# Kernel tuning notes

Measured on AMD Instinct MI355X. Metric: run time of the kernel, lower is better.

## Reference

```python
import jax, jax.numpy as jnp
import numpy as np

C_CONST = 8.0   # RG-LRU decay constant (Griffin/Hawk)
EPS = 1e-6      # RMSNorm eps
K = 4           # causal depthwise conv kernel size


def rmsnorm(x, w):
    # x: [B,S,D]
    var = jnp.mean(x * x, axis=-1, keepdims=True)
    return x * jax.lax.rsqrt(var + EPS) * w


def causal_depthwise_conv(x, conv_w, conv_b):
    # x: [B,S,D], conv_w: [K,D], conv_b: [D]; causal (left-pad K-1)
    B, S, D = x.shape
    xp = jnp.pad(x, ((0, 0), (K - 1, 0), (0, 0)))
    out = conv_b
    for k in range(K):  # tiny fixed loop over kernel taps
        out = out + conv_w[k] * xp[:, k:k + S, :]
    return out


def rg_lru(x, Wi, Wa, lam):
    # x: [B,S,D]; diagonal linear recurrence h_t = a_t*h_{t-1} + sqrt(1-a_t^2)*(i_t*x_t)
    r = jax.nn.sigmoid(jnp.einsum('bsd,de->bse', x, Wa))   # recurrence gate
    i = jax.nn.sigmoid(jnp.einsum('bsd,de->bse', x, Wi))   # input gate
    log_a = -C_CONST * jax.nn.softplus(lam) * r            # [B,S,D]
    a = jnp.exp(log_a)
    b = jnp.sqrt(jnp.maximum(1.0 - a * a, 1e-12)) * (i * x)

    def comb(e1, e2):
        a1, b1 = e1
        a2, b2 = e2
        return (a1 * a2, a2 * b1 + b2)

    _, h = jax.lax.associative_scan(comb, (a, b), axis=1)
    return h


def setup_inputs() -> dict:
    key = jax.random.key(0)
    ks = jax.random.split(key, 16)
    B, S, D, H = 4, 2048, 1024, 4096
    s = 0.02
    return {
        'x': jax.random.normal(ks[0], (B, S, D), jnp.float32),
        'norm1_w': jnp.ones((D,), jnp.float32),
        'Wx': jax.random.normal(ks[1], (D, D), jnp.float32) * s,
        'Wy': jax.random.normal(ks[2], (D, D), jnp.float32) * s,
        'conv_w': jax.random.normal(ks[3], (K, D), jnp.float32) * s,
        'conv_b': jnp.zeros((D,), jnp.float32),
        'Wi': jax.random.normal(ks[4], (D, D), jnp.float32) * s,
        'Wa': jax.random.normal(ks[5], (D, D), jnp.float32) * s,
        'lam': jax.random.normal(ks[6], (D,), jnp.float32) * 0.5,
        'Wo': jax.random.normal(ks[7], (D, D), jnp.float32) * s,
        'norm2_w': jnp.ones((D,), jnp.float32),
        'Wg': jax.random.normal(ks[8], (D, H), jnp.float32) * s,
        'Wu': jax.random.normal(ks[9], (D, H), jnp.float32) * s,
        'Wd': jax.random.normal(ks[10], (H, D), jnp.float32) * s,
    }


def reference(x, norm1_w, Wx, Wy, conv_w, conv_b, Wi, Wa, lam, Wo,
              norm2_w, Wg, Wu, Wd):
    # --- mixing block (Hawk recurrent block) with pre-norm + residual ---
    t = rmsnorm(x, norm1_w)
    xb = jnp.einsum('bsd,de->bse', t, Wx)          # recurrence branch
    xb = causal_depthwise_conv(xb, conv_w, conv_b)
    h = rg_lru(xb, Wi, Wa, lam)
    yb = jax.nn.gelu(jnp.einsum('bsd,de->bse', t, Wy))  # gate branch
    mix = jnp.einsum('bsd,de->bse', h * yb, Wo)
    h1 = x + mix
    # --- gated MLP with pre-norm + residual ---
    u = rmsnorm(h1, norm2_w)
    ffn = jnp.einsum('bsh,hd->bsd', jax.nn.gelu(jnp.einsum('bsd,dh->bsh', u, Wg)) * jnp.einsum('bsd,dh->bsh', u, Wu), Wd)
    return h1 + ffn
```

## Files before the change

kernel.cpp:

```cpp
#include <hip/hip_runtime.h>
#include <hip/hip_bf16.h>
#include <stdint.h>

#define B_SZ   4
#define S_LEN  2048
#define D_DIM  1024
#define H_DIM  4096
#define T_TOK  (B_SZ * S_LEN)
#define NC     64
#define CL     32

typedef unsigned short u16;
typedef unsigned int   u32;
typedef __attribute__((ext_vector_type(8))) short short8;
typedef __attribute__((ext_vector_type(4))) float f32x4;

__device__ __forceinline__ float tof(u16 u) {
    union { u32 i; float f; } v; v.i = ((u32)u) << 16; return v.f;
}
__device__ __forceinline__ u16 tobf(float f) {
    union { float f; u32 i; } v; v.f = f;
    u32 x = v.i;
    return (u16)((x + 0x7FFFu + ((x >> 16) & 1u)) >> 16);
}
__device__ __forceinline__ void unp8(uint4 v, float* f) {
    f[0] = tof(v.x & 0xffff); f[1] = tof(v.x >> 16);
    f[2] = tof(v.y & 0xffff); f[3] = tof(v.y >> 16);
    f[4] = tof(v.z & 0xffff); f[5] = tof(v.z >> 16);
    f[6] = tof(v.w & 0xffff); f[7] = tof(v.w >> 16);
}

__device__ __forceinline__ float gelu_f(float x) {
    float x3 = x * x * x;
    float tin = 0.7978845608028654f * (x + 0.044715f * x3);
    float e = __expf(2.f * tin);
    float th = 1.f - 2.f / (e + 1.f);
    return 0.5f * x * (1.f + th);
}
__device__ __forceinline__ float sig_f(float x) {
    return 1.f / (1.f + __expf(-x));
}

__device__ __forceinline__ void gload16(const void* g, void* l) {
    __builtin_amdgcn_global_load_lds(
        (const __attribute__((address_space(1))) u32*)g,
        (__attribute__((address_space(3))) u32*)l,
        16, 0, 0);
}

__global__ void detect_k(const u32* __restrict__ w, int* __restrict__ flag) {
    if (blockIdx.x == 0 && threadIdx.x == 0)
        *flag = (w[0] == 0x3F800000u) ? 1 : 0;
}

__global__ __launch_bounds__(256) void prep_small(
    const void* n1w, const void* n2w, const void* cw, const void* cb,
    const void* lam, u16* n1wc, u16* n2wc, u16* cwc, u16* cbc,
    float* acoef, const int* __restrict__ flagp) {
    int i = blockIdx.x * 256 + threadIdx.x;
    bool f32 = (*flagp) != 0;
    auto rd = [&](const void* p, int j) {
        return f32 ? ((const float*)p)[j] : tof(((const u16*)p)[j]);
    };
    if (i < 1024) n1wc[i] = tobf(rd(n1w, i));
    else if (i < 2048) n2wc[i - 1024] = tobf(rd(n2w, i - 1024));
    else if (i < 6144) cwc[i - 2048] = tobf(rd(cw, i - 2048));
    else if (i < 7168) cbc[i - 6144] = tobf(rd(cb, i - 6144));
    else {
        int d = i - 7168;
        float l = rd(lam, d);
        float sp = fmaxf(l, 0.f) + log1pf(__expf(-fabsf(l)));
        acoef[d] = -8.f * sp;
    }
}

__global__ __launch_bounds__(256) void transpose_any(
    const void* __restrict__ W, u16* __restrict__ WT, int R, int C,
    const int* __restrict__ flag) {
    __shared__ u16 tile[32][33];
    bool f32 = (*flag) != 0;
    int tx = threadIdx.x & 31, ty = threadIdx.x >> 5;
    int c0 = blockIdx.x * 32, r0 = blockIdx.y * 32;
#pragma unroll
    for (int k = 0; k < 4; k++) {
        size_t idx = (size_t)(r0 + ty + k * 8) * C + c0 + tx;
        tile[ty + k * 8][tx] = f32 ? tobf(((const float*)W)[idx])
                                   : ((const u16*)W)[idx];
    }
    __syncthreads();
#pragma unroll
    for (int k = 0; k < 4; k++)
        WT[(size_t)(c0 + ty + k * 8) * R + r0 + tx] = tile[tx][ty + k * 8];
}

__global__ __launch_bounds__(256) void transpose_ilv(
    const void* __restrict__ W, u16* __restrict__ WT, int R, int C, int par,
    const int* __restrict__ flag) {
    __shared__ u16 tile[32][33];
    bool f32 = (*flag) != 0;
    int tx = threadIdx.x & 31, ty = threadIdx.x >> 5;
    int c0 = blockIdx.x * 32, r0 = blockIdx.y * 32;
#pragma unroll
    for (int k = 0; k < 4; k++) {
        size_t idx = (size_t)(r0 + ty + k * 8) * C + c0 + tx;
        tile[ty + k * 8][tx] = f32 ? tobf(((const float*)W)[idx])
                                   : ((const u16*)W)[idx];
    }
    __syncthreads();
#pragma unroll
    for (int k = 0; k < 4; k++)
        WT[(size_t)(2 * (c0 + ty + k * 8) + par) * R + r0 + tx] =
            tile[tx][ty + k * 8];
}

__global__ __launch_bounds__(256) void rmsnorm_any(
    const void* __restrict__ X, const u16* __restrict__ Wt, u16* __restrict__ O,
    const int* __restrict__ flagp, int in_mode) {
    bool f32 = in_mode == 1 || (*flagp != 0);
    int row = blockIdx.x;
    int t = threadIdx.x;
    float x0, x1, x2, x3;
    if (f32) {
        float4 v = ((const float4*)((const float*)X + (size_t)row * D_DIM))[t];
        x0 = v.x; x1 = v.y; x2 = v.z; x3 = v.w;
    } else {
        uint2 pv = ((const uint2*)((const u16*)X + (size_t)row * D_DIM))[t];
        x0 = tof(pv.x & 0xffff); x1 = tof(pv.x >> 16);
        x2 = tof(pv.y & 0xffff); x3 = tof(pv.y >> 16);
    }
    float ss = x0 * x0 + x1 * x1 + x2 * x2 + x3 * x3;
#pragma unroll
    for (int off = 32; off; off >>= 1) ss += __shfl_down(ss, off, 64);
    __shared__ float red[4];
    if ((t & 63) == 0) red[t >> 6] = ss;
    __syncthreads();
    float tot = red[0] + red[1] + red[2] + red[3];
    float rs = rsqrtf(tot * (1.f / D_DIM) + 1e-6f);
    uint2 wv = ((const uint2*)Wt)[t];
    float w0 = tof(wv.x & 0xffff), w1 = tof(wv.x >> 16);
    float w2 = tof(wv.y & 0xffff), w3 = tof(wv.y >> 16);
    uint2 ov;
    ov.x = (u32)tobf(x0 * rs * w0) | ((u32)tobf(x1 * rs * w1) << 16);
    ov.y = (u32)tobf(x2 * rs * w2) | ((u32)tobf(x3 * rs * w3) << 16);
    ((uint2*)(O + (size_t)row * D_DIM))[t] = ov;
}

__global__ __launch_bounds__(256) void conv_k(
    const u16* __restrict__ xb, const u16* __restrict__ cw,
    const u16* __restrict__ cb, u16* __restrict__ xc) {
    size_t idx = (size_t)blockIdx.x * 256 + threadIdx.x;
    int dp = (int)(idx & 127);
    size_t ts = idx >> 7;
    int s = (int)(ts & (S_LEN - 1));
    int d0 = dp * 8;
    float acc[8];
    unp8(*(const uint4*)(cb + d0), acc);
    size_t base = ts * D_DIM + d0;
#pragma unroll
    for (int k = 0; k < 4; k++) {
        int sp = s + k - 3;
        if (sp >= 0) {
            float xf[8], wf[8];
            unp8(*(const uint4*)(xb + base + (ptrdiff_t)(k - 3) * D_DIM), xf);
            unp8(*(const uint4*)(cw + k * D_DIM + d0), wf);
#pragma unroll
            for (int e = 0; e < 8; e++) acc[e] += wf[e] * xf[e];
        }
    }
    uint4 ov;
    ov.x = (u32)tobf(acc[0]) | ((u32)tobf(acc[1]) << 16);
    ov.y = (u32)tobf(acc[2]) | ((u32)tobf(acc[3]) << 16);
    ov.z = (u32)tobf(acc[4]) | ((u32)tobf(acc[5]) << 16);
    ov.w = (u32)tobf(acc[6]) | ((u32)tobf(acc[7]) << 16);
    *(uint4*)(xc + base) = ov;
}

__global__ __launch_bounds__(256) void gates_chunk_k(
    const u16* __restrict__ r, const u16* __restrict__ ii, const u16* __restrict__ xc,
    const float* __restrict__ acoef, float2* __restrict__ Ap2, float2* __restrict__ Bs2) {
    int d2 = blockIdx.x * 256 + threadIdx.x;
    int c = blockIdx.y, b = blockIdx.z;
    float ac0 = acoef[d2 * 2], ac1 = acoef[d2 * 2 + 1];
    const u32* r2 = (const u32*)r;
    const u32* i2 = (const u32*)ii;
    const u32* x2 = (const u32*)xc;
    size_t base = ((size_t)b * S_LEN + c * CL) * (D_DIM / 2) + d2;
    float ap0 = 1.f, bs0 = 0.f, ap1 = 1.f, bs1 = 0.f;
    for (int tt = 0; tt < CL; tt++) {
        u32 rv = r2[base], iv = i2[base], xv = x2[base];
        float a0 = __expf(ac0 * tof(rv & 0xffff));
        float a1 = __expf(ac1 * tof(rv >> 16));
        float b0 = sqrtf(fmaxf(1.f - a0 * a0, 1e-12f)) * (tof(iv & 0xffff) * tof(xv & 0xffff));
        float b1 = sqrtf(fmaxf(1.f - a1 * a1, 1e-12f)) * (tof(iv >> 16) * tof(xv >> 16));
        ap0 *= a0; bs0 = fmaf(a0, bs0, b0);
        ap1 *= a1; bs1 = fmaf(a1, bs1, b1);
        base += D_DIM / 2;
    }
    size_t o = ((size_t)b * NC + c) * (D_DIM / 2) + d2;
    Ap2[o] = make_float2(ap0, ap1);
    Bs2[o] = make_float2(bs0, bs1);
}

__global__ __launch_bounds__(256) void carry_k(
    const float2* __restrict__ Ap2, const float2* __restrict__ Bs2,
    float2* __restrict__ carry2) {
    int d2 = blockIdx.x * 256 + threadIdx.x;
    int b = blockIdx.y;
    float2 h = make_float2(0.f, 0.f);
    for (int c = 0; c < NC; c++) {
        size_t o = ((size_t)b * NC + c) * (D_DIM / 2) + d2;
        float2 ap = Ap2[o], bs = Bs2[o];
        carry2[o] = h;
        h.x = fmaf(ap.x, h.x, bs.x);
        h.y = fmaf(ap.y, h.y, bs.y);
    }
}

__global__ __launch_bounds__(256) void apply_k(
    const u16* __restrict__ r, const u16* __restrict__ ii, const u16* __restrict__ xc,
    const float* __restrict__ acoef, const float2* __restrict__ carry2,
    const u16* __restrict__ yb, u16* __restrict__ g) {
    int d2 = blockIdx.x * 256 + threadIdx.x;
    int c = blockIdx.y, b = blockIdx.z;
    float ac0 = acoef[d2 * 2], ac1 = acoef[d2 * 2 + 1];
    float2 h = carry2[((size_t)b * NC + c) * (D_DIM / 2) + d2];
    const u32* r2 = (const u32*)r;
    const u32* i2 = (const u32*)ii;
    const u32* x2 = (const u32*)xc;
    const u32* y2 = (const u32*)yb;
    u32* g2 = (u32*)g;
    size_t base = ((size_t)b * S_LEN + c * CL) * (D_DIM / 2) + d2;
    for (int tt = 0; tt < CL; tt++) {
        u32 rv = r2[base], iv = i2[base], xv = x2[base], yv = y2[base];
        float a0 = __expf(ac0 * tof(rv & 0xffff));
        float a1 = __expf(ac1 * tof(rv >> 16));
        float b0 = sqrtf(fmaxf(1.f - a0 * a0, 1e-12f)) * (tof(iv & 0xffff) * tof(xv & 0xffff));
        float b1 = sqrtf(fmaxf(1.f - a1 * a1, 1e-12f)) * (tof(iv >> 16) * tof(xv >> 16));
        h.x = fmaf(a0, h.x, b0);
        h.y = fmaf(a1, h.y, b1);
        g2[base] = (u32)tobf(h.x * tof(yv & 0xffff)) |
                   ((u32)tobf(h.y * tof(yv >> 16)) << 16);
        base += D_DIM / 2;
    }
}

enum { EPI_NONE = 0, EPI_GELU = 1, EPI_SIG = 2, EPI_RESID = 3, EPI_MUL = 4 };

template <int E>
__device__ __forceinline__ float epi_apply(float v, const void* aux, size_t idx,
                                           bool auxF32) {
    if (E == EPI_GELU) return gelu_f(v);
    if (E == EPI_SIG) return sig_f(v);
    if (E == EPI_RESID) {
        float a = auxF32 ? ((const float*)aux)[idx] : tof(((const u16*)aux)[idx]);
        return v + a;
    }
    if (E == EPI_MUL) {
        float a = auxF32 ? ((const float*)aux)[idx] : tof(((const u16*)aux)[idx]);
        return v * a;
    }
    return v;
}

#define BK 64

template <int BM, int BN, int WMD, int WND, int EPI0, int EPI1, bool OUTF32,
          bool SWZ, bool GLU>
__global__ __launch_bounds__(WMD * WND * 64, 2) void gemm_db(
    const u16* __restrict__ A, const u16* __restrict__ BT,
    void* __restrict__ C0v, void* __restrict__ C1v, const void* __restrict__ aux,
    const int* __restrict__ flagp, int aux_mode,
    int M, int N, int K, int halfN) {
    constexpr int T  = WMD * WND * 64;
    constexpr int MR = BM / WMD;
    constexpr int NR = BN / WND;
    constexpr int MI = MR / 16;
    constexpr int NJ = NR / 16;
    constexpr int RPR = T / 8;

    __shared__ __align__(16) u16 As[2][BM * BK];
    __shared__ __align__(16) u16 Bs[2][BN * BK];

    const int t = threadIdx.x;
    const int lane = t & 63;
    const int w = t >> 6;
    const int wm = w / WND, wn = w % WND;
    const int quad = lane >> 4, l16 = lane & 15;

    int mt, nt;
    if (SWZ) {
        int GN = gridDim.x;
        int L = blockIdx.y * GN + blockIdx.x;
        int per = (GN * gridDim.y) >> 3;
        int id = (L & 7) * per + (L >> 3);
        mt = id / GN; nt = id - mt * GN;
    } else {
        mt = blockIdx.y; nt = blockIdx.x;
    }
    const int m0 = mt * BM;
    const int n0 = nt * BN;

    const int srow = t >> 3;
    const int cbg  = (t & 7) ^ (srow & 7);
    const u16* ag = A + (size_t)(m0 + srow) * K + cbg * 8;
    const u16* bg = BT + (size_t)(n0 + srow) * K + cbg * 8;
    const size_t rstep = (size_t)RPR * K;

    f32x4 acc[MI][NJ];
#pragma unroll
    for (int i = 0; i < MI; i++)
#pragma unroll
        for (int j = 0; j < NJ; j++) acc[i][j] = (f32x4){0.f, 0.f, 0.f, 0.f};

    const int r7 = l16 & 7;

    auto STAGE = [&](int s, int kt) {
        const u16* a = ag + (size_t)kt * BK;
        const u16* b = bg + (size_t)kt * BK;
        char* lA = (char*)&As[s][0] + t * 16;
        char* lB = (char*)&Bs[s][0] + t * 16;
#pragma unroll
        for (int rr = 0; rr < BM / RPR; rr++)
            gload16(a + rr * rstep, lA + rr * (RPR * 128));
#pragma unroll
        for (int rr = 0; rr < BN / RPR; rr++)
            gload16(b + rr * rstep, lB + rr * (RPR * 128));
    };
    auto COMPUTE = [&](int s) {
#pragma unroll
        for (int kk = 0; kk < 2; kk++) {
            const int cb = ((kk * 4 + quad) ^ r7) * 8;
            short8 af[MI], bf[NJ];
#pragma unroll
            for (int i = 0; i < MI; i++)
                af[i] = *(const short8*)&As[s][(wm * MR + i * 16 + l16) * BK + cb];
#pragma unroll
            for (int j = 0; j < NJ; j++)
                bf[j] = *(const short8*)&Bs[s][(wn * NR + j * 16 + l16) * BK + cb];
#pragma unroll
            for (int i = 0; i < MI; i++)
#pragma unroll
                for (int j = 0; j < NJ; j++)
                    acc[i][j] = __builtin_amdgcn_mfma_f32_16x16x32_bf16(
                        af[i], bf[j], acc[i][j], 0, 0, 0);
        }
    };

    const int NT = K >> 6;
    STAGE(0, 0);
    __syncthreads();
    for (int kt = 0; kt < NT; kt += 2) {
        STAGE(1, kt + 1);
        COMPUTE(0);
        __syncthreads();
        if (kt + 2 < NT) STAGE(0, kt + 2);
        COMPUTE(1);
        __syncthreads();
    }

    const bool auxF32 = (aux_mode == 2) || (aux_mode == 1 && *flagp != 0);
    const int side = (!GLU && n0 >= halfN) ? 1 : 0;
    void* Cv = side ? C1v : C0v;

#pragma unroll
    for (int i = 0; i < MI; i++) {
        int mbase = m0 + wm * MR + i * 16 + quad * 4;
#pragma unroll
        for (int j = 0; j < NJ; j++) {
            int ncol = n0 - side * halfN + wn * NR + j * 16 + l16;
#pragma unroll
            for (int rr = 0; rr < 4; rr++) {
                float v = acc[i][j][rr];
                if (GLU) {
                    float o = __shfl_xor(v, 1);
                    bool odd = (l16 & 1) != 0;
                    float gg = odd ? o : v;
                    float uu = odd ? v : o;
                    float res = gelu_f(gg) * uu;
                    if (!odd)
                        ((u16*)C0v)[(size_t)(mbase + rr) * halfN + (ncol >> 1)]
                            = tobf(res);
                } else {
                    size_t idx = (size_t)(mbase + rr) * halfN + ncol;
                    v = side ? epi_apply<EPI1>(v, aux, idx, auxF32)
                             : epi_apply<EPI0>(v, aux, idx, auxF32);
                    if (OUTF32) ((float*)Cv)[idx] = v;
                    else        ((u16*)Cv)[idx] = tobf(v);
                }
            }
        }
    }
}

extern "C" void kernel_launch(void* const* d_in, const int* in_sizes, int n_in,
                              void* d_out, int out_size, void* d_ws, size_t ws_size,
                              hipStream_t stream) {
    const void* x      = d_in[0];
    const void* n1w    = d_in[1];
    const void* Wx     = d_in[2];
    const void* Wy     = d_in[3];
    const void* conv_w = d_in[4];
    const void* conv_b = d_in[5];
    const void* Wi     = d_in[6];
    const void* Wa     = d_in[7];
    const void* lam    = d_in[8];
    const void* Wo     = d_in[9];
    const void* n2w    = d_in[10];
    const void* Wg     = d_in[11];
    const void* Wu     = d_in[12];
    const void* Wd     = d_in[13];
    float* out = (float*)d_out;

    char* ws = (char*)d_ws;
    auto alloc = [&](size_t bytes) {
        char* p = ws;
        ws += (bytes + 255) & ~(size_t)255;
        return p;
    };
    const size_t DD = (size_t)D_DIM * D_DIM;
    const size_t DH = (size_t)D_DIM * H_DIM * 2;
    const size_t TD = (size_t)T_TOK * D_DIM * 2;
    const size_t TH = (size_t)T_TOK * H_DIM * 2;

    int*  dflag  = (int*)alloc(256);
    u16*  n1wc   = (u16*)alloc(D_DIM * 2);
    u16*  n2wc   = (u16*)alloc(D_DIM * 2);
    u16*  cwc    = (u16*)alloc(4 * D_DIM * 2);
    u16*  cbc    = (u16*)alloc(D_DIM * 2);
    float* acoef = (float*)alloc(D_DIM * 4);
    float2* Ap2    = (float2*)alloc((size_t)B_SZ * NC * D_DIM * 4);
    float2* Bs2    = (float2*)alloc((size_t)B_SZ * NC * D_DIM * 4);
    float2* carry2 = (float2*)alloc((size_t)B_SZ * NC * D_DIM * 4);
    u16* WT  = (u16*)alloc(2 * DH);
    u16* T0  = (u16*)alloc(TD);
    u16* T1  = (u16*)alloc(TD);
    u16* T2  = (u16*)alloc(TD);
    u16* T3  = (u16*)alloc(TD);
    u16* T4  = (u16*)alloc(TD);
    u16* ggb = (u16*)alloc(TH);
    float* h1f = (float*)alloc((size_t)T_TOK * D_DIM * 4);

    dim3 b256(256);

    detect_k<<<dim3(1), dim3(64), 0, stream>>>((const u32*)n1w, dflag);
    prep_small<<<dim3(32), b256, 0, stream>>>(n1w, n2w, conv_w, conv_b, lam,
                                              n1wc, n2wc, cwc, cbc, acoef, dflag);

    rmsnorm_any<<<dim3(T_TOK), b256, 0, stream>>>(x, n1wc, T2, dflag, 0);

    transpose_any<<<dim3(32, 32), b256, 0, stream>>>(Wx, WT, D_DIM, D_DIM, dflag);
    transpose_any<<<dim3(32, 32), b256, 0, stream>>>(Wy, WT + DD, D_DIM, D_DIM, dflag);
    gemm_db<128, 128, 2, 2, EPI_NONE, EPI_GELU, false, false, false>
        <<<dim3(2 * D_DIM / 128, T_TOK / 128), b256, 0, stream>>>(
        T2, WT, T1, T3, nullptr, dflag, 0, T_TOK, 2 * D_DIM, D_DIM, D_DIM);

    conv_k<<<dim3(T_TOK * D_DIM / 8 / 256), b256, 0, stream>>>(T1, cwc, cbc, T0);

    transpose_any<<<dim3(32, 32), b256, 0, stream>>>(Wa, WT, D_DIM, D_DIM, dflag);
    transpose_any<<<dim3(32, 32), b256, 0, stream>>>(Wi, WT + DD, D_DIM, D_DIM, dflag);
    gemm_db<128, 128, 2, 2, EPI_SIG, EPI_SIG, false, false, false>
        <<<dim3(2 * D_DIM / 128, T_TOK / 128), b256, 0, stream>>>(
        T0, WT, T4, T2, nullptr, dflag, 0, T_TOK, 2 * D_DIM, D_DIM, D_DIM);

    gates_chunk_k<<<dim3(2, NC, B_SZ), b256, 0, stream>>>(T4, T2, T0, acoef, Ap2, Bs2);
    carry_k<<<dim3(2, B_SZ), b256, 0, stream>>>(Ap2, Bs2, carry2);
    apply_k<<<dim3(2, NC, B_SZ), b256, 0, stream>>>(T4, T2, T0, acoef, carry2, T3, T4);

    transpose_any<<<dim3(32, 32), b256, 0, stream>>>(Wo, WT, D_DIM, D_DIM, dflag);
    gemm_db<128, 128, 2, 2, EPI_RESID, EPI_RESID, true, false, false>
        <<<dim3(D_DIM / 128, T_TOK / 128), b256, 0, stream>>>(
        T4, WT, h1f, h1f, x, dflag, 1, T_TOK, D_DIM, D_DIM, D_DIM);

    rmsnorm_any<<<dim3(T_TOK), b256, 0, stream>>>(h1f, n2wc, T1, dflag, 1);

    transpose_ilv<<<dim3(H_DIM / 32, D_DIM / 32), b256, 0, stream>>>(
        Wg, WT, D_DIM, H_DIM, 0, dflag);
    transpose_ilv<<<dim3(H_DIM / 32, D_DIM / 32), b256, 0, stream>>>(
        Wu, WT, D_DIM, H_DIM, 1, dflag);
    gemm_db<128, 128, 2, 2, EPI_NONE, EPI_NONE, false, false, true>
        <<<dim3(2 * H_DIM / 128, T_TOK / 128), b256, 0, stream>>>(
        T1, WT, ggb, ggb, nullptr, dflag, 0, T_TOK, 2 * H_DIM, D_DIM, H_DIM);

    transpose_any<<<dim3(32, 128), b256, 0, stream>>>(Wd, WT, H_DIM, D_DIM, dflag);
    gemm_db<128, 128, 2, 2, EPI_RESID, EPI_RESID, true, true, false>
        <<<dim3(D_DIM / 128, T_TOK / 128), b256, 0, stream>>>(
        ggb, WT, out, out, h1f, dflag, 2, T_TOK, D_DIM, H_DIM, D_DIM);
}
```

Before: 685.9 us.

## Merge weight transposes into one launch and halve GEMM K-tile for higher occupancy

All eight weight transposes now run in a single launch that writes to separate workspace buffers, replacing eight small launches interleaved with the GEMMs. The GEMM K-tile drops from 64 to 32, with a new LDS swizzle and a single MFMA k-step per stage, which halves shared memory per block. Launch bounds are raised to 4 blocks per CU to use that. The cost is twice as many barriers and loop iterations per GEMM, less work per synchronisation, and possible register spills under the tighter bound.

```diff
diff --git a/kernel.cpp b/kernel.cpp
--- a/kernel.cpp
+++ b/kernel.cpp
@@ -74,13 +74,27 @@
     }
 }
 
-__global__ __launch_bounds__(256) void transpose_any(
-    const void* __restrict__ W, u16* __restrict__ WT, int R, int C,
-    const int* __restrict__ flag) {
+__global__ __launch_bounds__(256) void transpose_all(
+    const void* Wx_, const void* Wy_, const void* Wa_, const void* Wi_,
+    const void* Wo_, const void* Wd_, const void* Wg_, const void* Wu_,
+    u16* WTxy, u16* WTai, u16* WTo, u16* WTd, u16* WTgu,
+    const int* __restrict__ flagp) {
+    const size_t DD = (size_t)D_DIM * D_DIM;
+    bool f32 = (*flagp) != 0;
+    int b = blockIdx.x;
+    const void* W; u16* WT; int R, C, gx, ilv = 0, par = 0;
+    if (b < 1024)       { W = Wx_; WT = WTxy;      R = 1024; C = 1024; gx = 32;  b -= 0; }
+    else if (b < 2048)  { W = Wy_; WT = WTxy + DD; R = 1024; C = 1024; gx = 32;  b -= 1024; }
+    else if (b < 3072)  { W = Wa_; WT = WTai;      R = 1024; C = 1024; gx = 32;  b -= 2048; }
+    else if (b < 4096)  { W = Wi_; WT = WTai + DD; R = 1024; C = 1024; gx = 32;  b -= 3072; }
+    else if (b < 5120)  { W = Wo_; WT = WTo;       R = 1024; C = 1024; gx = 32;  b -= 4096; }
+    else if (b < 9216)  { W = Wd_; WT = WTd;       R = 4096; C = 1024; gx = 32;  b -= 5120; }
+    else if (b < 13312) { W = Wg_; WT = WTgu;      R = 1024; C = 4096; gx = 128; b -= 9216;  ilv = 1; par = 0; }
+    else                { W = Wu_; WT = WTgu;      R = 1024; C = 4096; gx = 128; b -= 13312; ilv = 1; par = 1; }
+    int bx = b % gx, by = b / gx;
     __shared__ u16 tile[32][33];
-    bool f32 = (*flag) != 0;
     int tx = threadIdx.x & 31, ty = threadIdx.x >> 5;
-    int c0 = blockIdx.x * 32, r0 = blockIdx.y * 32;
+    int c0 = bx * 32, r0 = by * 32;
 #pragma unroll
     for (int k = 0; k < 4; k++) {
         size_t idx = (size_t)(r0 + ty + k * 8) * C + c0 + tx;
@@ -89,28 +103,11 @@
     }
     __syncthreads();
 #pragma unroll
-    for (int k = 0; k < 4; k++)
-        WT[(size_t)(c0 + ty + k * 8) * R + r0 + tx] = tile[tx][ty + k * 8];
-}
-
-__global__ __launch_bounds__(256) void transpose_ilv(
-    const void* __restrict__ W, u16* __restrict__ WT, int R, int C, int par,
-    const int* __restrict__ flag) {
-    __shared__ u16 tile[32][33];
-    bool f32 = (*flag) != 0;
-    int tx = threadIdx.x & 31, ty = threadIdx.x >> 5;
-    int c0 = blockIdx.x * 32, r0 = blockIdx.y * 32;
-#pragma unroll
     for (int k = 0; k < 4; k++) {
-        size_t idx = (size_t)(r0 + ty + k * 8) * C + c0 + tx;
-        tile[ty + k * 8][tx] = f32 ? tobf(((const float*)W)[idx])
-                                   : ((const u16*)W)[idx];
-    }
-    __syncthreads();
-#pragma unroll
-    for (int k = 0; k < 4; k++)
-        WT[(size_t)(2 * (c0 + ty + k * 8) + par) * R + r0 + tx] =
-            tile[tx][ty + k * 8];
+        int cc = c0 + ty + k * 8;
+        size_t orow = ilv ? (size_t)(2 * cc + par) : (size_t)cc;
+        WT[orow * R + r0 + tx] = tile[tx][ty + k * 8];
+    }
 }
 
 __global__ __launch_bounds__(256) void rmsnorm_any(
@@ -262,11 +259,11 @@
     return v;
 }
 
-#define BK 64
+#define BK 32
 
 template <int BM, int BN, int WMD, int WND, int EPI0, int EPI1, bool OUTF32,
           bool SWZ, bool GLU>
-__global__ __launch_bounds__(WMD * WND * 64, 2) void gemm_db(
+__global__ __launch_bounds__(WMD * WND * 64, 4) void gemm_db(
     const u16* __restrict__ A, const u16* __restrict__ BT,
     void* __restrict__ C0v, void* __restrict__ C1v, const void* __restrict__ aux,
     const int* __restrict__ flagp, int aux_mode,
@@ -276,7 +273,7 @@
     constexpr int NR = BN / WND;
     constexpr int MI = MR / 16;
     constexpr int NJ = NR / 16;
-    constexpr int RPR = T / 8;
+    constexpr int RPR = T / 4;
 
     __shared__ __align__(16) u16 As[2][BM * BK];
     __shared__ __align__(16) u16 Bs[2][BN * BK];
@@ -300,8 +297,8 @@
     const int m0 = mt * BM;
     const int n0 = nt * BN;
 
-    const int srow = t >> 3;
-    const int cbg  = (t & 7) ^ (srow & 7);
+    const int srow = t >> 2;
+    const int cbg  = (t & 3) ^ ((srow >> 1) & 3);
     const u16* ag = A + (size_t)(m0 + srow) * K + cbg * 8;
     const u16* bg = BT + (size_t)(n0 + srow) * K + cbg * 8;
     const size_t rstep = (size_t)RPR * K;
@@ -312,7 +309,7 @@
 #pragma unroll
         for (int j = 0; j < NJ; j++) acc[i][j] = (f32x4){0.f, 0.f, 0.f, 0.f};
 
-    const int r7 = l16 & 7;
+    const int pcb = (quad ^ ((l16 >> 1) & 3)) * 8;
 
     auto STAGE = [&](int s, int kt) {
         const u16* a = ag + (size_t)kt * BK;
@@ -321,32 +318,28 @@
         char* lB = (char*)&Bs[s][0] + t * 16;
 #pragma unroll
         for (int rr = 0; rr < BM / RPR; rr++)
-            gload16(a + rr * rstep, lA + rr * (RPR * 128));
+            gload16(a + rr * rstep, lA + rr * (RPR * 64));
 #pragma unroll
         for (int rr = 0; rr < BN / RPR; rr++)
-            gload16(b + rr * rstep, lB + rr * (RPR * 128));
+            gload16(b + rr * rstep, lB + rr * (RPR * 64));
     };
     auto COMPUTE = [&](int s) {
-#pragma unroll
-        for (int kk = 0; kk < 2; kk++) {
-            const int cb = ((kk * 4 + quad) ^ r7) * 8;
-            short8 af[MI], bf[NJ];
-#pragma unroll
-            for (int i = 0; i < MI; i++)
-                af[i] = *(const short8*)&As[s][(wm * MR + i * 16 + l16) * BK + cb];
+        short8 af[MI], bf[NJ];
+#pragma unroll
+        for (int i = 0; i < MI; i++)
+            af[i] = *(const short8*)&As[s][(wm * MR + i * 16 + l16) * BK + pcb];
+#pragma unroll
+        for (int j = 0; j < NJ; j++)
+            bf[j] = *(const short8*)&Bs[s][(wn * NR + j * 16 + l16) * BK + pcb];
+#pragma unroll
+        for (int i = 0; i < MI; i++)
 #pragma unroll
             for (int j = 0; j < NJ; j++)
-                bf[j] = *(const short8*)&Bs[s][(wn * NR + j * 16 + l16) * BK + cb];
-#pragma unroll
-            for (int i = 0; i < MI; i++)
-#pragma unroll
-                for (int j = 0; j < NJ; j++)
-                    acc[i][j] = __builtin_amdgcn_mfma_f32_16x16x32_bf16(
-                        af[i], bf[j], acc[i][j], 0, 0, 0);
-        }
+                acc[i][j] = __builtin_amdgcn_mfma_f32_16x16x32_bf16(
+                    af[i], bf[j], acc[i][j], 0, 0, 0);
     };
 
-    const int NT = K >> 6;
+    const int NT = K >> 5;
     STAGE(0, 0);
     __syncthreads();
     for (int kt = 0; kt < NT; kt += 2) {
@@ -418,7 +411,6 @@
         return p;
     };
     const size_t DD = (size_t)D_DIM * D_DIM;
-    const size_t DH = (size_t)D_DIM * H_DIM * 2;
     const size_t TD = (size_t)T_TOK * D_DIM * 2;
     const size_t TH = (size_t)T_TOK * H_DIM * 2;
 
@@ -431,7 +423,11 @@
     float2* Ap2    = (float2*)alloc((size_t)B_SZ * NC * D_DIM * 4);
     float2* Bs2    = (float2*)alloc((size_t)B_SZ * NC * D_DIM * 4);
     float2* carry2 = (float2*)alloc((size_t)B_SZ * NC * D_DIM * 4);
-    u16* WT  = (u16*)alloc(2 * DH);
+    u16* WTxy = (u16*)alloc(2 * DD * 2);
+    u16* WTai = (u16*)alloc(2 * DD * 2);
+    u16* WTo  = (u16*)alloc(DD * 2);
+    u16* WTd  = (u16*)alloc((size_t)D_DIM * H_DIM * 2);
+    u16* WTgu = (u16*)alloc((size_t)D_DIM * H_DIM * 2 * 2);
     u16* T0  = (u16*)alloc(TD);
     u16* T1  = (u16*)alloc(TD);
     u16* T2  = (u16*)alloc(TD);
@@ -445,44 +441,36 @@
     detect_k<<<dim3(1), dim3(64), 0, stream>>>((const u32*)n1w, dflag);
     prep_small<<<dim3(32), b256, 0, stream>>>(n1w, n2w, conv_w, conv_b, lam,
                                               n1wc, n2wc, cwc, cbc, acoef, dflag);
+    transpose_all<<<dim3(17408), b256, 0, stream>>>(
+        Wx, Wy, Wa, Wi, Wo, Wd, Wg, Wu, WTxy, WTai, WTo, WTd, WTgu, dflag);
 
     rmsnorm_any<<<dim3(T_TOK), b256, 0, stream>>>(x, n1wc, T2, dflag, 0);
 
-    transpose_any<<<dim3(32, 32), b256, 0, stream>>>(Wx, WT, D_DIM, D_DIM, dflag);
-    transpose_any<<<dim3(32, 32), b256, 0, stream>>>(Wy, WT + DD, D_DIM, D_DIM, dflag);
     gemm_db<128, 128, 2, 2, EPI_NONE, EPI_GELU, false, false, false>
         <<<dim3(2 * D_DIM / 128, T_TOK / 128), b256, 0, stream>>>(
-        T2, WT, T1, T3, nullptr, dflag, 0, T_TOK, 2 * D_DIM, D_DIM, D_DIM);
+        T2, WTxy, T1, T3, nullptr, dflag, 0, T_TOK, 2 * D_DIM, D_DIM, D_DIM);
 
     conv_k<<<dim3(T_TOK * D_DIM / 8 / 256), b256, 0, stream>>>(T1, cwc, cbc, T0);
 
-    transpose_any<<<dim3(32, 32), b256, 0, stream>>>(Wa, WT, D_DIM, D_DIM, dflag);
-    transpose_any<<<dim3(32, 32), b256, 0, stream>>>(Wi, WT + DD, D_DIM, D_DIM, dflag);
     gemm_db<128, 128, 2, 2, EPI_SIG, EPI_SIG, false, false, false>
         <<<dim3(2 * D_DIM / 128, T_TOK / 128), b256, 0, stream>>>(
-        T0, WT, T4, T2, nullptr, dflag, 0, T_TOK, 2 * D_DIM, D_DIM, D_DIM);
+        T0, WTai, T4, T2, nullptr, dflag, 0, T_TOK, 2 * D_DIM, D_DIM, D_DIM);
 
     gates_chunk_k<<<dim3(2, NC, B_SZ), b256, 0, stream>>>(T4, T2, T0, acoef, Ap2, Bs2);
     carry_k<<<dim3(2, B_SZ), b256, 0, stream>>>(Ap2, Bs2, carry2);
     apply_k<<<dim3(2, NC, B_SZ), b256, 0, stream>>>(T4, T2, T0, acoef, carry2, T3, T4);
 
-    transpose_any<<<dim3(32, 32), b256, 0, stream>>>(Wo, WT, D_DIM, D_DIM, dflag);
     gemm_db<128, 128, 2, 2, EPI_RESID, EPI_RESID, true, false, false>
         <<<dim3(D_DIM / 128, T_TOK / 128), b256, 0, stream>>>(
-        T4, WT, h1f, h1f, x, dflag, 1, T_TOK, D_DIM, D_DIM, D_DIM);
+        T4, WTo, h1f, h1f, x, dflag, 1, T_TOK, D_DIM, D_DIM, D_DIM);
 
     rmsnorm_any<<<dim3(T_TOK), b256, 0, stream>>>(h1f, n2wc, T1, dflag, 1);
 
-    transpose_ilv<<<dim3(H_DIM / 32, D_DIM / 32), b256, 0, stream>>>(
-        Wg, WT, D_DIM, H_DIM, 0, dflag);
-    transpose_ilv<<<dim3(H_DIM / 32, D_DIM / 32), b256, 0, stream>>>(
-        Wu, WT, D_DIM, H_DIM, 1, dflag);
     gemm_db<128, 128, 2, 2, EPI_NONE, EPI_NONE, false, false, true>
         <<<dim3(2 * H_DIM / 128, T_TOK / 128), b256, 0, stream>>>(
-        T1, WT, ggb, ggb, nullptr, dflag, 0, T_TOK, 2 * H_DIM, D_DIM, H_DIM);
-
-    transpose_any<<<dim3(32, 128), b256, 0, stream>>>(Wd, WT, H_DIM, D_DIM, dflag);
+        T1, WTgu, ggb, ggb, nullptr, dflag, 0, T_TOK, 2 * H_DIM, D_DIM, H_DIM);
+
     gemm_db<128, 128, 2, 2, EPI_RESID, EPI_RESID, true, true, false>
         <<<dim3(D_DIM / 128, T_TOK / 128), b256, 0, stream>>>(
-        ggb, WT, out, out, h1f, dflag, 2, T_TOK, D_DIM, H_DIM, D_DIM);
-}
+        ggb, WTd, out, out, h1f, dflag, 2, T_TOK, D_DIM, H_DIM, D_DIM);
+}
```

After: 685.1 us. About the same (-0.1%).
